# Optimization experiments

Hardware: AMD Instinct MI355X
Metric: run time of the kernel (lower is better)

## Reference

```python
import jax, jax.numpy as jnp
import numpy as np

DIM = 64       # feature_dim
EDIM = 4       # edge_dim
EH = 128       # edge MLP hidden
MDIM = 64      # message dim


def _glorot(key, shape):
    fan_in = shape[0]
    return jax.random.normal(key, shape, dtype=jnp.float32) / jnp.sqrt(jnp.float32(fan_in))


def setup_inputs() -> dict:
    key = jax.random.key(0)
    ks = jax.random.split(key, 16)
    B, N = 8, 384
    feats = jax.random.normal(ks[0], (B, N, DIM), dtype=jnp.float32)
    coors = jax.random.normal(ks[1], (B, N, 3), dtype=jnp.float32)
    vel = jax.random.normal(ks[2], (B, N, 3), dtype=jnp.float32)
    edges = jax.random.normal(ks[3], (B, N, N, EDIM), dtype=jnp.float32)
    e_in = 2 * DIM + 1 + EDIM  # [h_i, h_j, ||x_i-x_j||^2, e_ij]
    params = dict(
        We1=_glorot(ks[4], (e_in, EH)), be1=jnp.zeros((EH,), jnp.float32),
        We2=_glorot(ks[5], (EH, MDIM)), be2=jnp.zeros((MDIM,), jnp.float32),
        Wc1=_glorot(ks[6], (MDIM, MDIM)), bc1=jnp.zeros((MDIM,), jnp.float32),
        Wc2=_glorot(ks[7], (MDIM, 1)), bc2=jnp.zeros((1,), jnp.float32),
        Wn1=_glorot(ks[8], (DIM + MDIM, 2 * DIM)), bn1=jnp.zeros((2 * DIM,), jnp.float32),
        Wn2=_glorot(ks[9], (2 * DIM, DIM)), bn2=jnp.zeros((DIM,), jnp.float32),
        Wv=_glorot(ks[10], (DIM, 1)), bv=jnp.zeros((1,), jnp.float32),
    )
    return dict(feats=feats, coors=coors, vel=vel, edges=edges, **params)


def _egnn(feats, coors, vel, edges, We1, be1, We2, be2, Wc1, bc1, Wc2, bc2,
          Wn1, bn1, Wn2, bn2, Wv, bv):
    B, N, _ = feats.shape
    # pairwise relative coordinates and squared distances
    rel = coors[:, :, None, :] - coors[:, None, :, :]            # [B,N,N,3]
    dist2 = jnp.sum(rel * rel, axis=-1, keepdims=True)           # [B,N,N,1]
    hi = jnp.broadcast_to(feats[:, :, None, :], (B, N, N, DIM))
    hj = jnp.broadcast_to(feats[:, None, :, :], (B, N, N, DIM))
    e_in = jnp.concatenate([hi, hj, dist2, edges], axis=-1)      # [B,N,N,2d+1+e]
    m = jax.nn.silu(e_in @ We1 + be1)
    m = jax.nn.silu(m @ We2 + be2)                                # [B,N,N,MDIM]
    # coordinate weights (scalar per edge)
    cw = jax.nn.silu(m @ Wc1 + bc1) @ Wc2 + bc2                   # [B,N,N,1]
    agg = jnp.mean(rel * cw, axis=2)                              # [B,N,3]
    # velocity update: vel' = phi_vel(h) * vel + agg ; coors' = coors + vel'
    gate = feats @ Wv + bv                                        # [B,N,1]
    vel_new = gate * vel + agg
    coors_new = coors + vel_new
    # node update with summed messages, residual
    m_i = jnp.sum(m, axis=2)                                      # [B,N,MDIM]
    h = jnp.concatenate([feats, m_i], axis=-1)
    h = jax.nn.silu(h @ Wn1 + bn1) @ Wn2 + bn2
    feats_new = feats + h
    return feats_new, coors_new, vel_new


def reference(feats, coors, vel, edges, We1, be1, We2, be2, Wc1, bc1, Wc2, bc2,
              Wn1, bn1, Wn2, bn2, Wv, bv):
    t, c, v = _egnn(feats, coors, vel, edges, We1, be1, We2, be2, Wc1, bc1,
                    Wc2, bc2, Wn1, bn1, Wn2, bn2, Wv, bv)
    return (t, jax.nn.selu(c), jax.nn.selu(v))
```

## Files before the change

kernel.cpp:

```cpp
#include <hip/hip_runtime.h>
#include <hip/hip_bf16.h>
#include <cstdint>

#define NN 384
#define OUT1OFF 196608
#define OUT2OFF 205824

typedef float f4 __attribute__((ext_vector_type(4)));
typedef short short8 __attribute__((ext_vector_type(8)));
typedef unsigned int u32;

union FragU { short8 s; u32 w[4]; };

__device__ inline unsigned short f2bf(float f) {
    u32 u = __float_as_uint(f);
    return (unsigned short)((u + 0x7fffu + ((u >> 16) & 1u)) >> 16);
}
__device__ inline u32 pkbf(float lo, float hi) {
    u32 r;
    asm("v_cvt_pk_bf16_f32 %0, %1, %2" : "=v"(r) : "v"(lo), "v"(hi));
    return r;
}
__device__ inline float siluf(float x) {
    return x * __builtin_amdgcn_rcpf(1.0f + __expf(-x));
}
__device__ inline float seluf(float x) {
    const float sc = 1.0507009873554805f, al = 1.6732632423543772f;
    return x > 0.f ? sc * x : sc * al * (__expf(x) - 1.f);
}

#define DSFENCE() do { asm volatile("s_waitcnt lgkmcnt(0)" ::: "memory"); \
                       __builtin_amdgcn_sched_barrier(0); } while (0)

__global__ __launch_bounds__(128) void egnn_prep1(
    const float* __restrict__ feats, const float* __restrict__ We1,
    const float* __restrict__ be1, float* __restrict__ HiC, float* __restrict__ HjC) {
    int r0 = blockIdx.x * 8;
    int t = threadIdx.x;
    __shared__ float fr[8][64];
    for (int k = t; k < 512; k += 128) fr[k >> 6][k & 63] = feats[(size_t)r0 * 64 + k];
    __syncthreads();
    float a1[8], a2[8];
#pragma unroll
    for (int r = 0; r < 8; r++) { a1[r] = be1[t]; a2[r] = 0.f; }
    for (int d = 0; d < 64; d++) {
        float w1 = We1[d * 128 + t], w2 = We1[(64 + d) * 128 + t];
#pragma unroll
        for (int r = 0; r < 8; r++) { a1[r] += fr[r][d] * w1; a2[r] += fr[r][d] * w2; }
    }
#pragma unroll
    for (int r = 0; r < 8; r++) {
        HiC[(size_t)(r0 + r) * 128 + t] = a1[r];
        HjC[(size_t)(r0 + r) * 128 + t] = a2[r];
    }
}

__global__ __launch_bounds__(64) void egnn_prep2(
    const float* __restrict__ We2, const float* __restrict__ Wc1,
    unsigned short* __restrict__ B2P, unsigned short* __restrict__ B3P) {
    int f = blockIdx.x;
    int l = threadIdx.x;
    int g = l >> 4, cc = l & 15;
    if (f < 16) {
        int n = f >> 2, ks = f & 3;
#pragma unroll
        for (int e = 0; e < 8; e++) {
            int row = ks * 32 + 8 * g + e, col = n * 16 + cc;
            B2P[(f * 64 + l) * 8 + e] = f2bf(We2[row * 64 + col]);
        }
    } else {
        int f2 = f - 16;
        int n = f2 >> 1, k2 = f2 & 1;
#pragma unroll
        for (int e = 0; e < 8; e++) {
            int row = k2 * 32 + 8 * g + e, col = n * 16 + cc;
            B3P[(f2 * 64 + l) * 8 + e] = f2bf(Wc1[row * 64 + col]);
        }
    }
}

__global__ __launch_bounds__(256, 3) void egnn_main(
    const float* __restrict__ feats, const float* __restrict__ coors,
    const float* __restrict__ vel, const float* __restrict__ edges,
    const float* __restrict__ We1,
    const float* __restrict__ be2, const float* __restrict__ bc1,
    const float* __restrict__ Wc2, const float* __restrict__ bc2,
    const float* __restrict__ Wn1, const float* __restrict__ bn1,
    const float* __restrict__ Wn2, const float* __restrict__ bn2,
    const float* __restrict__ Wv, const float* __restrict__ bv,
    const float* __restrict__ HiC, const float* __restrict__ HjC,
    const unsigned short* __restrict__ B2P, const unsigned short* __restrict__ B3P,
    float* __restrict__ out) {
    __shared__ __align__(16) unsigned short W2L[8192];
    __shared__ __align__(16) unsigned short W3L[4096];
    __shared__ __align__(16) short xch[4][16][136];
    __shared__ __align__(16) float red[4][128];
    __shared__ __align__(16) float hid[4][128];

    const int tid = threadIdx.x;
    const int w = tid >> 6, lane = tid & 63;
    const int g = lane >> 4, c = lane & 15;

    {
        const uint4* s2 = (const uint4*)B2P; uint4* dst2 = (uint4*)W2L;
        for (int k = tid; k < 1024; k += 256) dst2[k] = s2[k];
        const uint4* s3 = (const uint4*)B3P; uint4* dst3 = (uint4*)W3L;
        for (int k = tid; k < 512; k += 256) dst3[k] = s3[k];
    }

    const int flat = blockIdx.x * 4 + w;
    const int b = flat / NN;
    const size_t bi = (size_t)flat;

    red[w][lane] = HiC[bi * 128 + lane];
    red[w][64 + lane] = HiC[bi * 128 + 64 + lane];
    __syncthreads();

    u32 w1p0[8], w1p1[8], w1p2[8];
#pragma unroll
    for (int n = 0; n < 8; n++) {
        float v0 = 0.f, v1 = 0.f, v2 = 0.f, v3 = 0.f, v4 = 0.f;
        if (g == 0) {
            const int h = n * 16 + c;
            v0 = We1[128 * 128 + h]; v1 = We1[129 * 128 + h];
            v2 = We1[130 * 128 + h]; v3 = We1[131 * 128 + h];
            v4 = We1[132 * 128 + h];
        }
        w1p0[n] = pkbf(v0, v1);
        w1p1[n] = pkbf(v2, v3);
        w1p2[n] = pkbf(v4, 0.f);
    }

    f4 be2v[4], bc1v[4], wc2v[4];
#pragma unroll
    for (int n = 0; n < 4; n++) {
        be2v[n] = *(const f4*)&be2[n * 16 + 4 * g];
        bc1v[n] = *(const f4*)&bc1[n * 16 + 4 * g];
        wc2v[n] = *(const f4*)&Wc2[n * 16 + 4 * g];
    }
    const float bc2v = bc2[0];
    const float ci0 = coors[bi * 3], ci1 = coors[bi * 3 + 1], ci2 = coors[bi * 3 + 2];
    const float cig = (g == 0) ? ci0 : ((g == 1) ? ci1 : ci2);

    f4 maccv[4];
#pragma unroll
    for (int n = 0; n < 4; n++) maccv[n] = (f4){0.f, 0.f, 0.f, 0.f};
    float aggp = 0.f;

    short* xrow = &xch[w][c][0];
    const unsigned short* w2base = &W2L[lane * 8];
    const unsigned short* w3base = &W3L[lane * 8];
    const float* redw = &red[w][0];

#pragma unroll 1
    for (int jt = 0; jt < 24; ++jt) {
        const int j = jt * 16 + c;
        const float* cjp = &coors[((size_t)b * NN + j) * 3];
        const float cj0 = cjp[0], cj1 = cjp[1], cj2 = cjp[2];
        const f4 ev = *(const f4*)&edges[(bi * NN + j) * 4];
        const float* hjp = &HjC[((size_t)b * NN + j) * 128];
        f4 hjv[8];
#pragma unroll
        for (int n = 0; n < 8; n++) hjv[n] = *(const f4*)&hjp[n * 16 + 4 * g];
        const float r0 = ci0 - cj0, r1 = ci1 - cj1, r2 = ci2 - cj2;
        const float d2v = r0 * r0 + r1 * r1 + r2 * r2;

        FragU b1;
        b1.w[0] = (g == 0) ? pkbf(d2v, ev.x) : 0u;
        b1.w[1] = (g == 0) ? pkbf(ev.y, ev.z) : 0u;
        b1.w[2] = (g == 0) ? pkbf(ev.w, 0.f) : 0u;
        b1.w[3] = 0u;

#pragma unroll
        for (int n = 0; n < 8; n++) {
            FragU a1;
            a1.w[0] = w1p0[n]; a1.w[1] = w1p1[n]; a1.w[2] = w1p2[n]; a1.w[3] = 0u;
            const f4 hcn = *(const f4*)&redw[n * 16 + 4 * g];
            f4 d1 = __builtin_amdgcn_mfma_f32_16x16x32_bf16(a1.s, b1.s, hcn, 0, 0, 0);
            f4 p = d1 + hjv[n];
            const u32 lo = pkbf(siluf(p.x), siluf(p.y));
            const u32 hi = pkbf(siluf(p.z), siluf(p.w));
            *(uint2*)&xrow[n * 16 + 4 * g] = make_uint2(lo, hi);
        }
        DSFENCE();

        f4 c2[4];
#pragma unroll
        for (int n = 0; n < 4; n++) c2[n] = be2v[n];
#pragma unroll
        for (int ks = 0; ks < 4; ks++) {
            const short8 b2 = *(const short8*)&xrow[ks * 32 + 8 * g];
#pragma unroll
            for (int n = 0; n < 4; n++) {
                const short8 wf = *(const short8*)&w2base[(n * 4 + ks) * 512];
                c2[n] = __builtin_amdgcn_mfma_f32_16x16x32_bf16(wf, b2, c2[n], 0, 0, 0);
            }
        }
#pragma unroll
        for (int n = 0; n < 4; n++) {
            f4 s2;
            s2.x = siluf(c2[n].x); s2.y = siluf(c2[n].y);
            s2.z = siluf(c2[n].z); s2.w = siluf(c2[n].w);
            maccv[n] += s2;
            *(uint2*)&xrow[n * 16 + 4 * g] = make_uint2(pkbf(s2.x, s2.y), pkbf(s2.z, s2.w));
        }
        DSFENCE();

        f4 c3[4];
#pragma unroll
        for (int n = 0; n < 4; n++) c3[n] = bc1v[n];
#pragma unroll
        for (int k2 = 0; k2 < 2; k2++) {
            const short8 b3 = *(const short8*)&xrow[k2 * 32 + 8 * g];
#pragma unroll
            for (int n = 0; n < 4; n++) {
                const short8 wf = *(const short8*)&w3base[(n * 2 + k2) * 512];
                c3[n] = __builtin_amdgcn_mfma_f32_16x16x32_bf16(wf, b3, c3[n], 0, 0, 0);
            }
        }
        float cwp = 0.f;
#pragma unroll
        for (int n = 0; n < 4; n++) {
            cwp += siluf(c3[n].x) * wc2v[n].x;
            cwp += siluf(c3[n].y) * wc2v[n].y;
            cwp += siluf(c3[n].z) * wc2v[n].z;
            cwp += siluf(c3[n].w) * wc2v[n].w;
        }
        cwp += __shfl_xor(cwp, 16);
        cwp += __shfl_xor(cwp, 32);
        const float cw = cwp + bc2v;
        const float cjg = (g == 0) ? cj0 : ((g == 1) ? cj1 : cj2);
        aggp += (cig - cjg) * cw;
    }

#pragma unroll
    for (int n = 0; n < 4; n++) {
#pragma unroll
        for (int r = 0; r < 4; r++) {
            float v = maccv[n][r];
            v += __shfl_xor(v, 1); v += __shfl_xor(v, 2);
            v += __shfl_xor(v, 4); v += __shfl_xor(v, 8);
            maccv[n][r] = v;
        }
    }
    const float fv = feats[bi * 64 + lane];
    float gp = fv * Wv[lane];
    gp += __shfl_xor(gp, 1);  gp += __shfl_xor(gp, 2);
    gp += __shfl_xor(gp, 4);  gp += __shfl_xor(gp, 8);
    gp += __shfl_xor(gp, 16); gp += __shfl_xor(gp, 32);
    const float sgate = gp + bv[0];

    float aggr = aggp;
    aggr += __shfl_xor(aggr, 1); aggr += __shfl_xor(aggr, 2);
    aggr += __shfl_xor(aggr, 4); aggr += __shfl_xor(aggr, 8);

    red[w][lane] = fv;
    if (c == 0) {
#pragma unroll
        for (int n = 0; n < 4; n++)
            *(f4*)&red[w][64 + n * 16 + 4 * g] = maccv[n];
    }
    DSFENCE();

    float a0 = bn1[lane], a1 = bn1[64 + lane];
#pragma unroll 4
    for (int k0 = 0; k0 < 128; k0 += 4) {
        const f4 rv = *(const f4*)&redw[k0];
#pragma unroll
        for (int kk = 0; kk < 4; kk++) {
            const float* wr = &Wn1[(size_t)(k0 + kk) * 128];
            a0 += rv[kk] * wr[lane];
            a1 += rv[kk] * wr[64 + lane];
        }
    }
    const float h0 = siluf(a0), h1 = siluf(a1);
    hid[w][lane] = h0;
    hid[w][64 + lane] = h1;
    DSFENCE();
    float o = bn2[lane];
    const float* hidw = &hid[w][0];
#pragma unroll 4
    for (int k0 = 0; k0 < 128; k0 += 4) {
        const f4 hv = *(const f4*)&hidw[k0];
#pragma unroll
        for (int kk = 0; kk < 4; kk++)
            o += hv[kk] * Wn2[(size_t)(k0 + kk) * 64 + lane];
    }
    out[bi * 64 + lane] = fv + o;

    if (c == 0 && g < 3) {
        const size_t base = bi * 3 + g;
        const float vn = sgate * vel[base] + aggr * (1.f / 384.f);
        const float cn = coors[base] + vn;
        out[OUT1OFF + base] = seluf(cn);
        out[OUT2OFF + base] = seluf(vn);
    }
}

extern "C" void kernel_launch(void* const* d_in, const int* in_sizes, int n_in,
                              void* d_out, int out_size, void* d_ws, size_t ws_size,
                              hipStream_t stream) {
    const float* feats = (const float*)d_in[0];
    const float* coors = (const float*)d_in[1];
    const float* vel   = (const float*)d_in[2];
    const float* edges = (const float*)d_in[3];
    const float* We1   = (const float*)d_in[4];
    const float* be1   = (const float*)d_in[5];
    const float* We2   = (const float*)d_in[6];
    const float* be2   = (const float*)d_in[7];
    const float* Wc1   = (const float*)d_in[8];
    const float* bc1   = (const float*)d_in[9];
    const float* Wc2   = (const float*)d_in[10];
    const float* bc2   = (const float*)d_in[11];
    const float* Wn1   = (const float*)d_in[12];
    const float* bn1   = (const float*)d_in[13];
    const float* Wn2   = (const float*)d_in[14];
    const float* bn2   = (const float*)d_in[15];
    const float* Wv    = (const float*)d_in[16];
    const float* bv    = (const float*)d_in[17];

    float* HiC = (float*)d_ws;
    float* HjC = HiC + 393216;
    unsigned short* B2P = (unsigned short*)(HjC + 393216);
    unsigned short* B3P = B2P + 8192;
    float* out = (float*)d_out;

    egnn_prep1<<<384, 128, 0, stream>>>(feats, We1, be1, HiC, HjC);
    egnn_prep2<<<24, 64, 0, stream>>>(We2, Wc1, B2P, B3P);
    egnn_main<<<768, 256, 0, stream>>>(feats, coors, vel, edges, We1,
                                       be2, bc1, Wc2, bc2, Wn1, bn1, Wn2, bn2,
                                       Wv, bv, HiC, HjC, B2P, B3P, out);
}
```

Measured before the change: 127.8 us.

## Keep MLP weight fragments in registers and fold hi bias into MFMA

Packed bf16 weight fragments for the second and third edge-MLP layers are now loaded once into registers, replacing the block-wide LDS staging and the per-tile LDS reads. The per-node hi term is folded into the first MFMA as an extra K column (bias row times a constant 1 in the B fragment), so hj becomes the accumulator and the separate add and LDS read go away. The red/hid LDS buffers alias the xch buffer and the __syncthreads is removed, cutting LDS use. Bias and Wc2 vectors are now reloaded from global memory each iteration. The extra fragment registers could limit occupancy under the 3-blocks launch bound.

```diff
diff --git a/kernel.cpp b/kernel.cpp
--- a/kernel.cpp
+++ b/kernel.cpp
@@ -91,53 +91,44 @@
     const float* __restrict__ HiC, const float* __restrict__ HjC,
     const unsigned short* __restrict__ B2P, const unsigned short* __restrict__ B3P,
     float* __restrict__ out) {
-    __shared__ __align__(16) unsigned short W2L[8192];
-    __shared__ __align__(16) unsigned short W3L[4096];
     __shared__ __align__(16) short xch[4][16][136];
-    __shared__ __align__(16) float red[4][128];
-    __shared__ __align__(16) float hid[4][128];
 
     const int tid = threadIdx.x;
     const int w = tid >> 6, lane = tid & 63;
     const int g = lane >> 4, c = lane & 15;
 
-    {
-        const uint4* s2 = (const uint4*)B2P; uint4* dst2 = (uint4*)W2L;
-        for (int k = tid; k < 1024; k += 256) dst2[k] = s2[k];
-        const uint4* s3 = (const uint4*)B3P; uint4* dst3 = (uint4*)W3L;
-        for (int k = tid; k < 512; k += 256) dst3[k] = s3[k];
-    }
-
     const int flat = blockIdx.x * 4 + w;
     const int b = flat / NN;
     const size_t bi = (size_t)flat;
 
-    red[w][lane] = HiC[bi * 128 + lane];
-    red[w][64 + lane] = HiC[bi * 128 + 64 + lane];
-    __syncthreads();
+    short8 b2f[4][4], b3f[4][2];
+#pragma unroll
+    for (int n = 0; n < 4; n++)
+#pragma unroll
+        for (int ks = 0; ks < 4; ks++)
+            b2f[n][ks] = *(const short8*)(B2P + ((n * 4 + ks) * 64 + lane) * 8);
+#pragma unroll
+    for (int n = 0; n < 4; n++)
+#pragma unroll
+        for (int k2 = 0; k2 < 2; k2++)
+            b3f[n][k2] = *(const short8*)(B3P + ((n * 2 + k2) * 64 + lane) * 8);
 
     u32 w1p0[8], w1p1[8], w1p2[8];
 #pragma unroll
     for (int n = 0; n < 8; n++) {
-        float v0 = 0.f, v1 = 0.f, v2 = 0.f, v3 = 0.f, v4 = 0.f;
+        float v0 = 0.f, v1 = 0.f, v2 = 0.f, v3 = 0.f, v4 = 0.f, v5 = 0.f;
         if (g == 0) {
             const int h = n * 16 + c;
             v0 = We1[128 * 128 + h]; v1 = We1[129 * 128 + h];
             v2 = We1[130 * 128 + h]; v3 = We1[131 * 128 + h];
             v4 = We1[132 * 128 + h];
+            v5 = HiC[bi * 128 + h];
         }
         w1p0[n] = pkbf(v0, v1);
         w1p1[n] = pkbf(v2, v3);
-        w1p2[n] = pkbf(v4, 0.f);
-    }
-
-    f4 be2v[4], bc1v[4], wc2v[4];
-#pragma unroll
-    for (int n = 0; n < 4; n++) {
-        be2v[n] = *(const f4*)&be2[n * 16 + 4 * g];
-        bc1v[n] = *(const f4*)&bc1[n * 16 + 4 * g];
-        wc2v[n] = *(const f4*)&Wc2[n * 16 + 4 * g];
-    }
+        w1p2[n] = pkbf(v4, v5);
+    }
+
     const float bc2v = bc2[0];
     const float ci0 = coors[bi * 3], ci1 = coors[bi * 3 + 1], ci2 = coors[bi * 3 + 2];
     const float cig = (g == 0) ? ci0 : ((g == 1) ? ci1 : ci2);
@@ -148,9 +139,6 @@
     float aggp = 0.f;
 
     short* xrow = &xch[w][c][0];
-    const unsigned short* w2base = &W2L[lane * 8];
-    const unsigned short* w3base = &W3L[lane * 8];
-    const float* redw = &red[w][0];
 
 #pragma unroll 1
     for (int jt = 0; jt < 24; ++jt) {
@@ -168,33 +156,29 @@
         FragU b1;
         b1.w[0] = (g == 0) ? pkbf(d2v, ev.x) : 0u;
         b1.w[1] = (g == 0) ? pkbf(ev.y, ev.z) : 0u;
-        b1.w[2] = (g == 0) ? pkbf(ev.w, 0.f) : 0u;
+        b1.w[2] = (g == 0) ? pkbf(ev.w, 1.0f) : 0u;
         b1.w[3] = 0u;
 
 #pragma unroll
         for (int n = 0; n < 8; n++) {
             FragU a1;
             a1.w[0] = w1p0[n]; a1.w[1] = w1p1[n]; a1.w[2] = w1p2[n]; a1.w[3] = 0u;
-            const f4 hcn = *(const f4*)&redw[n * 16 + 4 * g];
-            f4 d1 = __builtin_amdgcn_mfma_f32_16x16x32_bf16(a1.s, b1.s, hcn, 0, 0, 0);
-            f4 p = d1 + hjv[n];
-            const u32 lo = pkbf(siluf(p.x), siluf(p.y));
-            const u32 hi = pkbf(siluf(p.z), siluf(p.w));
+            f4 d1 = __builtin_amdgcn_mfma_f32_16x16x32_bf16(a1.s, b1.s, hjv[n], 0, 0, 0);
+            const u32 lo = pkbf(siluf(d1.x), siluf(d1.y));
+            const u32 hi = pkbf(siluf(d1.z), siluf(d1.w));
             *(uint2*)&xrow[n * 16 + 4 * g] = make_uint2(lo, hi);
         }
         DSFENCE();
 
         f4 c2[4];
 #pragma unroll
-        for (int n = 0; n < 4; n++) c2[n] = be2v[n];
+        for (int n = 0; n < 4; n++) c2[n] = *(const f4*)&be2[n * 16 + 4 * g];
 #pragma unroll
         for (int ks = 0; ks < 4; ks++) {
             const short8 b2 = *(const short8*)&xrow[ks * 32 + 8 * g];
 #pragma unroll
-            for (int n = 0; n < 4; n++) {
-                const short8 wf = *(const short8*)&w2base[(n * 4 + ks) * 512];
-                c2[n] = __builtin_amdgcn_mfma_f32_16x16x32_bf16(wf, b2, c2[n], 0, 0, 0);
-            }
+            for (int n = 0; n < 4; n++)
+                c2[n] = __builtin_amdgcn_mfma_f32_16x16x32_bf16(b2f[n][ks], b2, c2[n], 0, 0, 0);
         }
 #pragma unroll
         for (int n = 0; n < 4; n++) {
@@ -208,23 +192,22 @@
 
         f4 c3[4];
 #pragma unroll
-        for (int n = 0; n < 4; n++) c3[n] = bc1v[n];
+        for (int n = 0; n < 4; n++) c3[n] = *(const f4*)&bc1[n * 16 + 4 * g];
 #pragma unroll
         for (int k2 = 0; k2 < 2; k2++) {
             const short8 b3 = *(const short8*)&xrow[k2 * 32 + 8 * g];
 #pragma unroll
-            for (int n = 0; n < 4; n++) {
-                const short8 wf = *(const short8*)&w3base[(n * 2 + k2) * 512];
-                c3[n] = __builtin_amdgcn_mfma_f32_16x16x32_bf16(wf, b3, c3[n], 0, 0, 0);
-            }
+            for (int n = 0; n < 4; n++)
+                c3[n] = __builtin_amdgcn_mfma_f32_16x16x32_bf16(b3f[n][k2], b3, c3[n], 0, 0, 0);
         }
         float cwp = 0.f;
 #pragma unroll
         for (int n = 0; n < 4; n++) {
-            cwp += siluf(c3[n].x) * wc2v[n].x;
-            cwp += siluf(c3[n].y) * wc2v[n].y;
-            cwp += siluf(c3[n].z) * wc2v[n].z;
-            cwp += siluf(c3[n].w) * wc2v[n].w;
+            const f4 wc = *(const f4*)&Wc2[n * 16 + 4 * g];
+            cwp += siluf(c3[n].x) * wc.x;
+            cwp += siluf(c3[n].y) * wc.y;
+            cwp += siluf(c3[n].z) * wc.z;
+            cwp += siluf(c3[n].w) * wc.w;
         }
         cwp += __shfl_xor(cwp, 16);
         cwp += __shfl_xor(cwp, 32);
@@ -232,6 +215,10 @@
         const float cjg = (g == 0) ? cj0 : ((g == 1) ? cj1 : cj2);
         aggp += (cig - cjg) * cw;
     }
+
+    DSFENCE();
+    float* red = (float*)&xch[w][0][0];
+    float* hid = red + 128;
 
 #pragma unroll
     for (int n = 0; n < 4; n++) {
@@ -254,18 +241,18 @@
     aggr += __shfl_xor(aggr, 1); aggr += __shfl_xor(aggr, 2);
     aggr += __shfl_xor(aggr, 4); aggr += __shfl_xor(aggr, 8);
 
-    red[w][lane] = fv;
+    red[lane] = fv;
     if (c == 0) {
 #pragma unroll
         for (int n = 0; n < 4; n++)
-            *(f4*)&red[w][64 + n * 16 + 4 * g] = maccv[n];
+            *(f4*)&red[64 + n * 16 + 4 * g] = maccv[n];
     }
     DSFENCE();
 
     float a0 = bn1[lane], a1 = bn1[64 + lane];
 #pragma unroll 4
     for (int k0 = 0; k0 < 128; k0 += 4) {
-        const f4 rv = *(const f4*)&redw[k0];
+        const f4 rv = *(const f4*)&red[k0];
 #pragma unroll
         for (int kk = 0; kk < 4; kk++) {
             const float* wr = &Wn1[(size_t)(k0 + kk) * 128];
@@ -273,15 +260,13 @@
             a1 += rv[kk] * wr[64 + lane];
         }
     }
-    const float h0 = siluf(a0), h1 = siluf(a1);
-    hid[w][lane] = h0;
-    hid[w][64 + lane] = h1;
+    hid[lane] = siluf(a0);
+    hid[64 + lane] = siluf(a1);
     DSFENCE();
     float o = bn2[lane];
-    const float* hidw = &hid[w][0];
 #pragma unroll 4
     for (int k0 = 0; k0 < 128; k0 += 4) {
-        const f4 hv = *(const f4*)&hidw[k0];
+        const f4 hv = *(const f4*)&hid[k0];
 #pragma unroll
         for (int kk = 0; kk < 4; kk++)
             o += hv[kk] * Wn2[(size_t)(k0 + kk) * 64 + lane];
```

After: 249.5 us. 1.95x slower.
